# Performance work log

Measured on AMD Instinct MI355X. Metric: run time of the kernel, lower is better.

## Reference

```python
import jax, jax.numpy as jnp
import numpy as np

N = 50000
E = 400000
IN_C = 512
HID = 64
OUT_C = 40
H = 4
NEG_SLOPE = 0.2
EPS = 1e-16  # PyG softmax denominator epsilon


def glorot(key, shape, fan_in, fan_out):
    limit = float(np.sqrt(6.0 / (fan_in + fan_out)))
    return jax.random.uniform(key, shape, jnp.float32, -limit, limit)


def setup_inputs() -> dict:
    key = jax.random.key(0)
    ks = jax.random.split(key, 8)
    x = jax.random.normal(ks[0], (N, IN_C), jnp.float32)
    # random edges guaranteed to have src != dst (forward adds exactly one self-loop per node)
    src = jax.random.randint(ks[1], (E,), 0, N)
    off = jax.random.randint(ks[2], (E,), 1, N)
    dst = (src + off) % N
    edge_index = jnp.stack([src, dst], axis=0).astype(jnp.int64)
    W1 = glorot(ks[3], (IN_C, H * HID), IN_C, H * HID)
    b1 = jnp.zeros((H * HID,), jnp.float32)
    W2 = glorot(ks[4], (H * HID, H * OUT_C), H * HID, H * OUT_C)
    b2 = jnp.zeros((OUT_C,), jnp.float32)
    return {"x": x, "edge_index": edge_index, "W1": W1, "b1": b1, "W2": W2, "b2": b2}


def _supergat_layer(x, src, dst, W, b, heads, out_c, concat):
    n = x.shape[0]
    h = (x @ W).reshape(n, heads, out_c)            # [N,H,C]
    x_i = h[dst]                                    # [E',H,C] target
    x_j = h[src]                                    # [E',H,C] source
    # MX attention with return_logits=True inside message(): plain dot-product logits
    alpha = jnp.sum(x_i * x_j, axis=-1)             # [E',H]
    alpha = jax.nn.leaky_relu(alpha, NEG_SLOPE)
    # segment softmax over destination node
    amax = jax.ops.segment_max(alpha, dst, num_segments=n)
    alpha = jnp.exp(alpha - amax[dst])
    denom = jax.ops.segment_sum(alpha, dst, num_segments=n)
    alpha = alpha / (denom[dst] + EPS)
    out = jax.ops.segment_sum(x_j * alpha[:, :, None], dst, num_segments=n)  # [N,H,C]
    if concat:
        out = out.reshape(n, heads * out_c)
    else:
        out = out.mean(axis=1)
    return out + b


def reference(x, edge_index, W1, b1, W2, b2):
    # add_self_loops (input edges contain no self loops by construction)
    loop = jnp.arange(N, dtype=edge_index.dtype)
    src = jnp.concatenate([edge_index[0], loop])
    dst = jnp.concatenate([edge_index[1], loop])
    h = _supergat_layer(x, src, dst, W1, b1, H, HID, concat=True)
    h = jax.nn.elu(h)
    out = _supergat_layer(h, src, dst, W2, b2, H, OUT_C, concat=False)
    logp = jax.nn.log_softmax(out, axis=-1)
    att_loss = jnp.zeros((1,), jnp.float32)  # eval mode: get_attention_loss returns 0
    return logp, att_loss
```

## Files before the change

### kernel.cpp

```cpp
#include <hip/hip_runtime.h>
#include <cstddef>
#include <cstdint>

#define HEADS 4
#define OUTC  40
#define NEG   0.2f
#define EPSV  1e-16f

typedef __bf16 bf16x8 __attribute__((ext_vector_type(8)));
typedef float  floatx4 __attribute__((ext_vector_type(4)));

__device__ __forceinline__ void split_bf16(float a, unsigned& hi, unsigned& lo) {
  unsigned u = __float_as_uint(a);
  hi = u >> 16;
  float hf = __uint_as_float(u & 0xFFFF0000u);
  lo = __float_as_uint(a - hf) >> 16;
}

__device__ __forceinline__ void dma16(const void* g, void* l) {
  __builtin_amdgcn_global_load_lds(
      (const __attribute__((address_space(1))) unsigned int*)g,
      (__attribute__((address_space(3))) unsigned int*)l, 16, 0, 0);
}

__global__ void hist_k(const int* __restrict__ dst, int* __restrict__ cnt, int E) {
  int e = blockIdx.x * blockDim.x + threadIdx.x;
  if (e < E) atomicAdd(&cnt[dst[e]], 1);
}

__global__ __launch_bounds__(1024) void scanA_k(const int* __restrict__ cnt,
                                                int* __restrict__ rp,
                                                int* __restrict__ bsum, int n) {
  __shared__ int sh[1024];
  int i = blockIdx.x * 1024 + threadIdx.x;
  int v = (i < n) ? cnt[i] : 0;
  sh[threadIdx.x] = v;
  __syncthreads();
  for (int d = 1; d < 1024; d <<= 1) {
    int t = (threadIdx.x >= d) ? sh[threadIdx.x - d] : 0;
    __syncthreads();
    sh[threadIdx.x] += t;
    __syncthreads();
  }
  if (i < n) rp[i] = sh[threadIdx.x] - v;
  if (threadIdx.x == 1023) bsum[blockIdx.x] = sh[1023];
}

__global__ void scanC_k(int* __restrict__ rp, const int* __restrict__ bsum,
                        int n, int nb) {
  int i = blockIdx.x * blockDim.x + threadIdx.x;
  if (i < n) {
    int b = i >> 10;
    int off = 0;
    for (int j = 0; j < b; ++j) off += bsum[j];
    rp[i] += off;
  }
  if (i == 0) {
    int tot = 0;
    for (int j = 0; j < nb; ++j) tot += bsum[j];
    rp[n] = tot;
  }
}

__global__ void scatter_k(const int* __restrict__ src, const int* __restrict__ dst,
                          const int* __restrict__ rp, int* __restrict__ cur,
                          int* __restrict__ out, int E) {
  int e = blockIdx.x * blockDim.x + threadIdx.x;
  if (e < E) {
    int d = dst[e];
    int p = rp[d] + atomicAdd(&cur[d], 1);
    out[p] = src[e];
  }
}

__global__ void convW_k(const float* __restrict__ W1, unsigned short* __restrict__ Wh1,
                        unsigned short* __restrict__ Wl1,
                        const float* __restrict__ W2, unsigned short* __restrict__ Wh2,
                        unsigned short* __restrict__ Wl2) {
  int id = blockIdx.x * 256 + threadIdx.x;
  if (id < 256 * 512) {
    int n = id >> 9, k = id & 511;
    unsigned h, l;
    split_bf16(W1[k * 256 + n], h, l);
    Wh1[id] = (unsigned short)h;
    Wl1[id] = (unsigned short)l;
  } else {
    int id2 = id - 256 * 512;
    int n = id2 >> 8, k = id2 & 255;
    int hh = n >> 6, c = n & 63;
    float a = (c < OUTC) ? W2[k * 160 + hh * OUTC + c] : 0.f;
    unsigned h, l;
    split_bf16(a, h, l);
    Wh2[id2] = (unsigned short)h;
    Wl2[id2] = (unsigned short)l;
  }
}

template <bool A_FP32, bool COMPACT>
__global__ __launch_bounds__(256) void gemm_dma(const void* Aptr_h, const void* Aptr_l,
                                                const unsigned short* __restrict__ Bh,
                                                const unsigned short* __restrict__ Bl,
                                                float* __restrict__ C, int M, int K) {
  __shared__ __align__(16) unsigned char lds[65536];
  const int tid = threadIdx.x;
  const int lane = tid & 63;
  const int w = tid >> 6;
  const int wr = w >> 1, wc = w & 1;
  const int row0 = blockIdx.y * 128;
  const int col0 = blockIdx.x * 128;
  const int fr = lane & 15, fq = lane >> 4;

  floatx4 acc[4][4];
#pragma unroll
  for (int i = 0; i < 4; ++i)
#pragma unroll
    for (int j = 0; j < 4; ++j) acc[i][j] = (floatx4){0.f, 0.f, 0.f, 0.f};

  const float* Af32 = (const float*)Aptr_h;
  const unsigned short* Agh = (const unsigned short*)Aptr_h;
  const unsigned short* Agl = (const unsigned short*)Aptr_l;

#define DMA_TILE(K0, BASE)                                                          \
  do {                                                                              \
    if (A_FP32) {                                                                   \
      _Pragma("unroll") for (int t = 0; t < 4; ++t) {                               \
        int arow = w * 32 + t * 8 + (lane >> 3);                                    \
        int gr = row0 + arow; gr = gr < M ? gr : M - 1;                             \
        dma16(&Af32[(size_t)gr * K + (K0) + (lane & 7) * 4],                        \
              lds + (BASE) + (size_t)(w * 32 + t * 8) * 128);                       \
      }                                                                             \
    } else {                                                                        \
      _Pragma("unroll") for (int t = 0; t < 2; ++t) {                               \
        int arow = w * 32 + t * 16 + (lane >> 2);                                   \
        int gr = row0 + arow; gr = gr < M ? gr : M - 1;                             \
        size_t go = (size_t)gr * K + (K0) + (lane & 3) * 8;                         \
        dma16(&Agh[go], lds + (BASE) + (size_t)(w * 32 + t * 16) * 64);             \
        dma16(&Agl[go], lds + (BASE) + 8192 + (size_t)(w * 32 + t * 16) * 64);      \
      }                                                                             \
    }                                                                               \
    _Pragma("unroll") for (int t = 0; t < 2; ++t) {                                 \
      int nrow = w * 32 + t * 16 + (lane >> 2);                                     \
      size_t go = (size_t)(col0 + nrow) * K + (K0) + (lane & 3) * 8;                \
      dma16(&Bh[go], lds + (BASE) + 16384 + (size_t)(w * 32 + t * 16) * 64);        \
      dma16(&Bl[go], lds + (BASE) + 24576 + (size_t)(w * 32 + t * 16) * 64);        \
    }                                                                               \
  } while (0)

  const int nk = K >> 5;
  DMA_TILE(0, 0);
  for (int k = 0; k < nk; ++k) {
    const int cur = (k & 1) << 15;
    if (k + 1 < nk) {
      DMA_TILE((k + 1) << 5, ((k + 1) & 1) << 15);
      asm volatile("s_waitcnt vmcnt(8)" ::: "memory");
    } else {
      asm volatile("s_waitcnt vmcnt(0)" ::: "memory");
    }
    asm volatile("s_barrier" ::: "memory");

    bf16x8 ah[4], al[4], bh[4], bl[4];
#pragma unroll
    for (int i = 0; i < 4; ++i) {
      int arow = wr * 64 + i * 16 + fr;
      if (A_FP32) {
        const float* pr = (const float*)(lds + cur + (size_t)arow * 128 + fq * 32);
        float4 v0 = *(const float4*)pr;
        float4 v1 = *(const float4*)(pr + 4);
        unsigned u0 = __float_as_uint(v0.x), u1 = __float_as_uint(v0.y);
        unsigned u2 = __float_as_uint(v0.z), u3 = __float_as_uint(v0.w);
        unsigned u4 = __float_as_uint(v1.x), u5 = __float_as_uint(v1.y);
        unsigned u6 = __float_as_uint(v1.z), u7 = __float_as_uint(v1.w);
        uint4 H;
        H.x = (u0 >> 16) | (u1 & 0xFFFF0000u);
        H.y = (u2 >> 16) | (u3 & 0xFFFF0000u);
        H.z = (u4 >> 16) | (u5 & 0xFFFF0000u);
        H.w = (u6 >> 16) | (u7 & 0xFFFF0000u);
        uint4 L;
        L.x = (__float_as_uint(v0.x - __uint_as_float(u0 & 0xFFFF0000u)) >> 16) |
              (__float_as_uint(v0.y - __uint_as_float(u1 & 0xFFFF0000u)) & 0xFFFF0000u);
        L.y = (__float_as_uint(v0.z - __uint_as_float(u2 & 0xFFFF0000u)) >> 16) |
              (__float_as_uint(v0.w - __uint_as_float(u3 & 0xFFFF0000u)) & 0xFFFF0000u);
        L.z = (__float_as_uint(v1.x - __uint_as_float(u4 & 0xFFFF0000u)) >> 16) |
              (__float_as_uint(v1.y - __uint_as_float(u5 & 0xFFFF0000u)) & 0xFFFF0000u);
        L.w = (__float_as_uint(v1.z - __uint_as_float(u6 & 0xFFFF0000u)) >> 16) |
              (__float_as_uint(v1.w - __uint_as_float(u7 & 0xFFFF0000u)) & 0xFFFF0000u);
        ah[i] = *(bf16x8*)&H;
        al[i] = *(bf16x8*)&L;
      } else {
        ah[i] = *(bf16x8*)(lds + cur + (size_t)arow * 64 + fq * 16);
        al[i] = *(bf16x8*)(lds + cur + 8192 + (size_t)arow * 64 + fq * 16);
      }
      int brow = wc * 64 + i * 16 + fr;
      bh[i] = *(bf16x8*)(lds + cur + 16384 + (size_t)brow * 64 + fq * 16);
      bl[i] = *(bf16x8*)(lds + cur + 24576 + (size_t)brow * 64 + fq * 16);
    }
#pragma unroll
    for (int i = 0; i < 4; ++i)
#pragma unroll
      for (int j = 0; j < 4; ++j) {
        acc[i][j] = __builtin_amdgcn_mfma_f32_16x16x32_bf16(ah[i], bh[j], acc[i][j], 0, 0, 0);
        acc[i][j] = __builtin_amdgcn_mfma_f32_16x16x32_bf16(ah[i], bl[j], acc[i][j], 0, 0, 0);
        acc[i][j] = __builtin_amdgcn_mfma_f32_16x16x32_bf16(al[i], bh[j], acc[i][j], 0, 0, 0);
      }
    asm volatile("s_barrier" ::: "memory");
  }
#undef DMA_TILE

#pragma unroll
  for (int i = 0; i < 4; ++i) {
    int grow_base = row0 + wr * 64 + i * 16 + fq * 4;
#pragma unroll
    for (int r = 0; r < 4; ++r) {
      int grow = grow_base + r;
      if (grow < M) {
        if (COMPACT) {
          int head = blockIdx.x * 2 + wc;
#pragma unroll
          for (int j = 0; j < 4; ++j) {
            int cc = j * 16 + fr;
            if (cc < OUTC) C[(size_t)grow * 160 + head * OUTC + cc] = acc[i][j][r];
          }
        } else {
#pragma unroll
          for (int j = 0; j < 4; ++j)
            C[(size_t)grow * 256 + col0 + wc * 64 + j * 16 + fr] = acc[i][j][r];
        }
      }
    }
  }
}

__global__ __launch_bounds__(256) void agg1_k(const float* __restrict__ h,
                                              const int* __restrict__ rp,
                                              const int* __restrict__ srt,
                                              const float* __restrict__ b1,
                                              unsigned short* __restrict__ outh,
                                              unsigned short* __restrict__ outl, int Nn) {
  int wv = threadIdx.x >> 6, lane = threadIdx.x & 63;
  int node = blockIdx.x * 4 + wv;
  if (node >= Nn) node = Nn - 1;
  const float4 xi = *(const float4*)&h[(size_t)node * 256 + lane * 4];
  float p = xi.x * xi.x + xi.y * xi.y + xi.z * xi.z + xi.w * xi.w;
  p += __shfl_xor(p, 1); p += __shfl_xor(p, 2); p += __shfl_xor(p, 4); p += __shfl_xor(p, 8);
  float a = p > 0.f ? p : NEG * p;
  float m = a, l = 1.f;
  float4 acc = xi;
  const int e0 = rp[node], e1 = rp[node + 1];
  for (int e = e0; e < e1; ++e) {
    int s = srt[e];
    const float4 xj = *(const float4*)&h[(size_t)s * 256 + lane * 4];
    float q = xi.x * xj.x + xi.y * xj.y + xi.z * xj.z + xi.w * xj.w;
    q += __shfl_xor(q, 1); q += __shfl_xor(q, 2); q += __shfl_xor(q, 4); q += __shfl_xor(q, 8);
    float al = q > 0.f ? q : NEG * q;
    float nm = fmaxf(m, al);
    float sc = __expf(m - nm), wt = __expf(al - nm);
    l = l * sc + wt;
    acc.x = acc.x * sc + wt * xj.x;
    acc.y = acc.y * sc + wt * xj.y;
    acc.z = acc.z * sc + wt * xj.z;
    acc.w = acc.w * sc + wt * xj.w;
    m = nm;
  }
  float inv = 1.f / (l + EPSV);
  const float4 bb = *(const float4*)&b1[lane * 4];
  float4 o;
  o.x = acc.x * inv + bb.x;
  o.y = acc.y * inv + bb.y;
  o.z = acc.z * inv + bb.z;
  o.w = acc.w * inv + bb.w;
  o.x = o.x > 0.f ? o.x : __expf(o.x) - 1.f;
  o.y = o.y > 0.f ? o.y : __expf(o.y) - 1.f;
  o.z = o.z > 0.f ? o.z : __expf(o.z) - 1.f;
  o.w = o.w > 0.f ? o.w : __expf(o.w) - 1.f;
  unsigned h0, l0, h1, l1, h2, l2, h3, l3;
  split_bf16(o.x, h0, l0);
  split_bf16(o.y, h1, l1);
  split_bf16(o.z, h2, l2);
  split_bf16(o.w, h3, l3);
  size_t base = (size_t)node * 256 + lane * 4;
  *(uint2*)&outh[base] = make_uint2(h0 | (h1 << 16), h2 | (h3 << 16));
  *(uint2*)&outl[base] = make_uint2(l0 | (l1 << 16), l2 | (l3 << 16));
}

__global__ __launch_bounds__(256) void agg2_k(const float* __restrict__ h,
                                              const int* __restrict__ rp,
                                              const int* __restrict__ srt,
                                              const float* __restrict__ b2,
                                              float* __restrict__ out, int Nn) {
  __shared__ float buf[4][160];
  int wv = threadIdx.x >> 6, lane = threadIdx.x & 63;
  int node = blockIdx.x * 4 + wv;
  if (node >= Nn) node = Nn - 1;
  const int head = lane >> 4, c4 = lane & 15;
  const bool act = c4 < 10;
  float4 xi = make_float4(0.f, 0.f, 0.f, 0.f);
  if (act) xi = *(const float4*)&h[(size_t)node * 160 + head * OUTC + c4 * 4];
  float p = xi.x * xi.x + xi.y * xi.y + xi.z * xi.z + xi.w * xi.w;
  p += __shfl_xor(p, 1); p += __shfl_xor(p, 2); p += __shfl_xor(p, 4); p += __shfl_xor(p, 8);
  float a = p > 0.f ? p : NEG * p;
  float m = a, l = 1.f;
  float4 acc = xi;
  const int e0 = rp[node], e1 = rp[node + 1];
  for (int e = e0; e < e1; ++e) {
    int s = srt[e];
    float4 xj = make_float4(0.f, 0.f, 0.f, 0.f);
    if (act) xj = *(const float4*)&h[(size_t)s * 160 + head * OUTC + c4 * 4];
    float q = xi.x * xj.x + xi.y * xj.y + xi.z * xj.z + xi.w * xj.w;
    q += __shfl_xor(q, 1); q += __shfl_xor(q, 2); q += __shfl_xor(q, 4); q += __shfl_xor(q, 8);
    float al = q > 0.f ? q : NEG * q;
    float nm = fmaxf(m, al);
    float sc = __expf(m - nm), wt = __expf(al - nm);
    l = l * sc + wt;
    acc.x = acc.x * sc + wt * xj.x;
    acc.y = acc.y * sc + wt * xj.y;
    acc.z = acc.z * sc + wt * xj.z;
    acc.w = acc.w * sc + wt * xj.w;
    m = nm;
  }
  float inv = 1.f / (l + EPSV);
  if (act) {
    float4 res;
    res.x = acc.x * inv; res.y = acc.y * inv; res.z = acc.z * inv; res.w = acc.w * inv;
    *(float4*)&buf[wv][head * OUTC + c4 * 4] = res;
  }
  __syncthreads();
  const bool valid = lane < OUTC;
  float v = 0.f;
  if (valid)
    v = 0.25f * (buf[wv][lane] + buf[wv][OUTC + lane] + buf[wv][2 * OUTC + lane] +
                 buf[wv][3 * OUTC + lane]) + b2[lane];
  float t = valid ? v : -1e30f;
#pragma unroll
  for (int off = 32; off; off >>= 1) t = fmaxf(t, __shfl_xor(t, off));
  float ex = valid ? __expf(v - t) : 0.f;
  float s = ex;
#pragma unroll
  for (int off = 32; off; off >>= 1) s += __shfl_xor(s, off);
  float lse = t + __logf(s);
  if (valid) out[(size_t)node * OUTC + lane] = v - lse;
  if (blockIdx.x == 0 && threadIdx.x == 0) out[(size_t)Nn * OUTC] = 0.f;
}

extern "C" void kernel_launch(void* const* d_in, const int* in_sizes, int n_in,
                              void* d_out, int out_size, void* d_ws, size_t ws_size,
                              hipStream_t stream) {
  const float* x  = (const float*)d_in[0];
  const int*   ei = (const int*)d_in[1];
  const float* W1 = (const float*)d_in[2];
  const float* b1 = (const float*)d_in[3];
  const float* W2 = (const float*)d_in[4];
  const float* b2 = (const float*)d_in[5];
  float* out = (float*)d_out;

  const int Nn = in_sizes[0] / 512;
  const int E  = in_sizes[1] / 2;
  const int* esrc = ei;
  const int* edst = ei + E;
  const int NB = (Nn + 1023) / 1024;

  char* ws = (char*)d_ws;
  const size_t szH = (size_t)Nn * 256 * sizeof(float);
  float* h1 = (float*)(ws);
  size_t off = szH;
  unsigned short* g1h = (unsigned short*)(ws + off); off += (size_t)Nn * 256 * 2;
  unsigned short* g1l = (unsigned short*)(ws + off); off += (size_t)Nn * 256 * 2;
  int* rp = (int*)(ws + off);   off += ((size_t)(Nn + 1) * 4 + 15) & ~(size_t)15;
  int* cnt = (int*)(ws + off);  off += ((size_t)Nn * 4 + 15) & ~(size_t)15;
  int* srt = (int*)(ws + off);  off += ((size_t)E * 4 + 15) & ~(size_t)15;
  int* bsum = (int*)(ws + off); off += 1024;
  unsigned short* Wh1 = (unsigned short*)(ws + off); off += (size_t)256 * 512 * 2;
  unsigned short* Wl1 = (unsigned short*)(ws + off); off += (size_t)256 * 512 * 2;
  unsigned short* Wh2 = (unsigned short*)(ws + off); off += (size_t)256 * 256 * 2;
  unsigned short* Wl2 = (unsigned short*)(ws + off); off += (size_t)256 * 256 * 2;
  float* h2 = h1;

  hipMemsetAsync(cnt, 0, (size_t)Nn * sizeof(int), stream);
  hist_k<<<(E + 255) / 256, 256, 0, stream>>>(edst, cnt, E);
  scanA_k<<<NB, 1024, 0, stream>>>(cnt, rp, bsum, Nn);
  scanC_k<<<(Nn + 255) / 256, 256, 0, stream>>>(rp, bsum, Nn, NB);
  hipMemsetAsync(cnt, 0, (size_t)Nn * sizeof(int), stream);
  scatter_k<<<(E + 255) / 256, 256, 0, stream>>>(esrc, edst, rp, cnt, srt, E);

  convW_k<<<768, 256, 0, stream>>>(W1, Wh1, Wl1, W2, Wh2, Wl2);

  gemm_dma<true, false>
      <<<dim3(2, (Nn + 127) / 128), 256, 0, stream>>>(x, nullptr, Wh1, Wl1, h1, Nn, 512);
  agg1_k<<<(Nn + 3) / 4, 256, 0, stream>>>(h1, rp, srt, b1, g1h, g1l, Nn);

  gemm_dma<false, true>
      <<<dim3(2, (Nn + 127) / 128), 256, 0, stream>>>(g1h, g1l, Wh2, Wl2, h2, Nn, 256);
  agg2_k<<<(Nn + 3) / 4, 256, 0, stream>>>(h2, rp, srt, b2, out, Nn);
}
```

Measured before the change: 427.4 us.

## Load GEMM A-operand directly to registers and unroll edge aggregation by two

The GEMM no longer stages the A tile through LDS. Each thread loads its A fragment straight from global memory into registers, and only B is double-buffered via DMA, which halves the LDS footprint and adds a launch-bounds occupancy hint of 3 blocks. Both aggregation kernels now process two neighbor edges per iteration with a combined online-softmax update, so two gathers are in flight at once. The risks are less coalesced global reads for A, higher register pressure, and vmcnt wait counts that depend on the exact number of loads issued.

Result: slower. 446.4 us (+4.5%).

```diff
diff --git a/kernel.cpp b/kernel.cpp
--- a/kernel.cpp
+++ b/kernel.cpp
@@ -97,11 +97,11 @@
 }
 
 template <bool A_FP32, bool COMPACT>
-__global__ __launch_bounds__(256) void gemm_dma(const void* Aptr_h, const void* Aptr_l,
-                                                const unsigned short* __restrict__ Bh,
-                                                const unsigned short* __restrict__ Bl,
-                                                float* __restrict__ C, int M, int K) {
-  __shared__ __align__(16) unsigned char lds[65536];
+__global__ __launch_bounds__(256, 3) void gemm_dma(const void* Aptr_h, const void* Aptr_l,
+                                                   const unsigned short* __restrict__ Bh,
+                                                   const unsigned short* __restrict__ Bl,
+                                                   float* __restrict__ C, int M, int K) {
+  __shared__ __align__(16) unsigned char lds[32768];
   const int tid = threadIdx.x;
   const int lane = tid & 63;
   const int w = tid >> 6;
@@ -120,52 +120,69 @@
   const unsigned short* Agh = (const unsigned short*)Aptr_h;
   const unsigned short* Agl = (const unsigned short*)Aptr_l;
 
-#define DMA_TILE(K0, BASE)                                                          \
+  size_t arow_off[4];
+#pragma unroll
+  for (int i = 0; i < 4; ++i) {
+    int gr = row0 + wr * 64 + i * 16 + fr;
+    gr = gr < M ? gr : M - 1;
+    arow_off[i] = (size_t)gr * K;
+  }
+
+#define DMA_B(K0, BASE)                                                             \
   do {                                                                              \
-    if (A_FP32) {                                                                   \
-      _Pragma("unroll") for (int t = 0; t < 4; ++t) {                               \
-        int arow = w * 32 + t * 8 + (lane >> 3);                                    \
-        int gr = row0 + arow; gr = gr < M ? gr : M - 1;                             \
-        dma16(&Af32[(size_t)gr * K + (K0) + (lane & 7) * 4],                        \
-              lds + (BASE) + (size_t)(w * 32 + t * 8) * 128);                       \
-      }                                                                             \
-    } else {                                                                        \
-      _Pragma("unroll") for (int t = 0; t < 2; ++t) {                               \
-        int arow = w * 32 + t * 16 + (lane >> 2);                                   \
-        int gr = row0 + arow; gr = gr < M ? gr : M - 1;                             \
-        size_t go = (size_t)gr * K + (K0) + (lane & 3) * 8;                         \
-        dma16(&Agh[go], lds + (BASE) + (size_t)(w * 32 + t * 16) * 64);             \
-        dma16(&Agl[go], lds + (BASE) + 8192 + (size_t)(w * 32 + t * 16) * 64);      \
-      }                                                                             \
-    }                                                                               \
     _Pragma("unroll") for (int t = 0; t < 2; ++t) {                                 \
       int nrow = w * 32 + t * 16 + (lane >> 2);                                     \
       size_t go = (size_t)(col0 + nrow) * K + (K0) + (lane & 3) * 8;                \
-      dma16(&Bh[go], lds + (BASE) + 16384 + (size_t)(w * 32 + t * 16) * 64);        \
-      dma16(&Bl[go], lds + (BASE) + 24576 + (size_t)(w * 32 + t * 16) * 64);        \
+      dma16(&Bh[go], lds + (BASE) + (size_t)(w * 32 + t * 16) * 64);                \
+      dma16(&Bl[go], lds + (BASE) + 8192 + (size_t)(w * 32 + t * 16) * 64);         \
     }                                                                               \
   } while (0)
 
   const int nk = K >> 5;
-  DMA_TILE(0, 0);
+  DMA_B(0, 0);
+  asm volatile("" ::: "memory");
   for (int k = 0; k < nk; ++k) {
-    const int cur = (k & 1) << 15;
+    const int cur = (k & 1) << 14;
+    const int k0 = k << 5;
+
+    float4 a0[4], a1[4];
+    bf16x8 ah[4], al[4];
+    if (A_FP32) {
+#pragma unroll
+      for (int i = 0; i < 4; ++i) {
+        const float* p = &Af32[arow_off[i] + k0 + fq * 8];
+        a0[i] = *(const float4*)p;
+        a1[i] = *(const float4*)(p + 4);
+      }
+    } else {
+#pragma unroll
+      for (int i = 0; i < 4; ++i) {
+        size_t go = arow_off[i] + k0 + fq * 8;
+        ah[i] = *(const bf16x8*)&Agh[go];
+        al[i] = *(const bf16x8*)&Agl[go];
+      }
+    }
+
     if (k + 1 < nk) {
-      DMA_TILE((k + 1) << 5, ((k + 1) & 1) << 15);
+      DMA_B((k + 1) << 5, ((k + 1) & 1) << 14);
+      asm volatile("s_waitcnt vmcnt(12)" ::: "memory");
+    } else {
       asm volatile("s_waitcnt vmcnt(8)" ::: "memory");
-    } else {
-      asm volatile("s_waitcnt vmcnt(0)" ::: "memory");
     }
     asm volatile("s_barrier" ::: "memory");
 
-    bf16x8 ah[4], al[4], bh[4], bl[4];
-#pragma unroll
-    for (int i = 0; i < 4; ++i) {
-      int arow = wr * 64 + i * 16 + fr;
-      if (A_FP32) {
-        const float* pr = (const float*)(lds + cur + (size_t)arow * 128 + fq * 32);
-        float4 v0 = *(const float4*)pr;
-        float4 v1 = *(const float4*)(pr + 4);
+    bf16x8 bh[4], bl[4];
+#pragma unroll
+    for (int j = 0; j < 4; ++j) {
+      int brow = wc * 64 + j * 16 + fr;
+      bh[j] = *(bf16x8*)(lds + cur + (size_t)brow * 64 + fq * 16);
+      bl[j] = *(bf16x8*)(lds + cur + 8192 + (size_t)brow * 64 + fq * 16);
+    }
+
+    if (A_FP32) {
+#pragma unroll
+      for (int i = 0; i < 4; ++i) {
+        float4 v0 = a0[i], v1 = a1[i];
         unsigned u0 = __float_as_uint(v0.x), u1 = __float_as_uint(v0.y);
         unsigned u2 = __float_as_uint(v0.z), u3 = __float_as_uint(v0.w);
         unsigned u4 = __float_as_uint(v1.x), u5 = __float_as_uint(v1.y);
@@ -186,14 +203,9 @@
               (__float_as_uint(v1.w - __uint_as_float(u7 & 0xFFFF0000u)) & 0xFFFF0000u);
         ah[i] = *(bf16x8*)&H;
         al[i] = *(bf16x8*)&L;
-      } else {
-        ah[i] = *(bf16x8*)(lds + cur + (size_t)arow * 64 + fq * 16);
-        al[i] = *(bf16x8*)(lds + cur + 8192 + (size_t)arow * 64 + fq * 16);
       }
-      int brow = wc * 64 + i * 16 + fr;
-      bh[i] = *(bf16x8*)(lds + cur + 16384 + (size_t)brow * 64 + fq * 16);
-      bl[i] = *(bf16x8*)(lds + cur + 24576 + (size_t)brow * 64 + fq * 16);
-    }
+    }
+
 #pragma unroll
     for (int i = 0; i < 4; ++i)
 #pragma unroll
@@ -204,7 +216,7 @@
       }
     asm volatile("s_barrier" ::: "memory");
   }
-#undef DMA_TILE
+#undef DMA_B
 
 #pragma unroll
   for (int i = 0; i < 4; ++i) {
@@ -246,7 +258,29 @@
   float m = a, l = 1.f;
   float4 acc = xi;
   const int e0 = rp[node], e1 = rp[node + 1];
-  for (int e = e0; e < e1; ++e) {
+  int e = e0;
+  for (; e + 2 <= e1; e += 2) {
+    int s0 = srt[e], s1 = srt[e + 1];
+    const float4 xj0 = *(const float4*)&h[(size_t)s0 * 256 + lane * 4];
+    const float4 xj1 = *(const float4*)&h[(size_t)s1 * 256 + lane * 4];
+    float q0 = xi.x * xj0.x + xi.y * xj0.y + xi.z * xj0.z + xi.w * xj0.w;
+    float q1 = xi.x * xj1.x + xi.y * xj1.y + xi.z * xj1.z + xi.w * xj1.w;
+    q0 += __shfl_xor(q0, 1); q1 += __shfl_xor(q1, 1);
+    q0 += __shfl_xor(q0, 2); q1 += __shfl_xor(q1, 2);
+    q0 += __shfl_xor(q0, 4); q1 += __shfl_xor(q1, 4);
+    q0 += __shfl_xor(q0, 8); q1 += __shfl_xor(q1, 8);
+    float a0 = q0 > 0.f ? q0 : NEG * q0;
+    float a1 = q1 > 0.f ? q1 : NEG * q1;
+    float nm = fmaxf(m, fmaxf(a0, a1));
+    float sc = __expf(m - nm), w0 = __expf(a0 - nm), w1 = __expf(a1 - nm);
+    l = l * sc + w0 + w1;
+    acc.x = acc.x * sc + w0 * xj0.x + w1 * xj1.x;
+    acc.y = acc.y * sc + w0 * xj0.y + w1 * xj1.y;
+    acc.z = acc.z * sc + w0 * xj0.z + w1 * xj1.z;
+    acc.w = acc.w * sc + w0 * xj0.w + w1 * xj1.w;
+    m = nm;
+  }
+  if (e < e1) {
     int s = srt[e];
     const float4 xj = *(const float4*)&h[(size_t)s * 256 + lane * 4];
     float q = xi.x * xj.x + xi.y * xj.y + xi.z * xj.z + xi.w * xj.w;
@@ -301,7 +335,33 @@
   float m = a, l = 1.f;
   float4 acc = xi;
   const int e0 = rp[node], e1 = rp[node + 1];
-  for (int e = e0; e < e1; ++e) {
+  int e = e0;
+  for (; e + 2 <= e1; e += 2) {
+    int s0 = srt[e], s1 = srt[e + 1];
+    float4 xj0 = make_float4(0.f, 0.f, 0.f, 0.f);
+    float4 xj1 = make_float4(0.f, 0.f, 0.f, 0.f);
+    if (act) {
+      xj0 = *(const float4*)&h[(size_t)s0 * 160 + head * OUTC + c4 * 4];
+      xj1 = *(const float4*)&h[(size_t)s1 * 160 + head * OUTC + c4 * 4];
+    }
+    float q0 = xi.x * xj0.x + xi.y * xj0.y + xi.z * xj0.z + xi.w * xj0.w;
+    float q1 = xi.x * xj1.x + xi.y * xj1.y + xi.z * xj1.z + xi.w * xj1.w;
+    q0 += __shfl_xor(q0, 1); q1 += __shfl_xor(q1, 1);
+    q0 += __shfl_xor(q0, 2); q1 += __shfl_xor(q1, 2);
+    q0 += __shfl_xor(q0, 4); q1 += __shfl_xor(q1, 4);
+    q0 += __shfl_xor(q0, 8); q1 += __shfl_xor(q1, 8);
+    float a0 = q0 > 0.f ? q0 : NEG * q0;
+    float a1 = q1 > 0.f ? q1 : NEG * q1;
+    float nm = fmaxf(m, fmaxf(a0, a1));
+    float sc = __expf(m - nm), w0 = __expf(a0 - nm), w1 = __expf(a1 - nm);
+    l = l * sc + w0 + w1;
+    acc.x = acc.x * sc + w0 * xj0.x + w1 * xj1.x;
+    acc.y = acc.y * sc + w0 * xj0.y + w1 * xj1.y;
+    acc.z = acc.z * sc + w0 * xj0.z + w1 * xj1.z;
+    acc.w = acc.w * sc + w0 * xj0.w + w1 * xj1.w;
+    m = nm;
+  }
+  if (e < e1) {
     int s = srt[e];
     float4 xj = make_float4(0.f, 0.f, 0.f, 0.f);
     if (act) xj = *(const float4*)&h[(size_t)s * 160 + head * OUTC + c4 * 4];
```
